# Optimization experiments

Hardware: AMD Instinct MI355X
Metric: run time of the kernel (lower is better)

The kernel has to match this reference:

```python
import jax, jax.numpy as jnp
import numpy as np

B, T, C = 2, 2048, 2048
H, D = 16, 128


def _rope(x, cos, sin):
    # x: [B,H,T,D], cos/sin: [T,D//2]
    half = x.shape[-1] // 2
    x1, x2 = x[..., :half], x[..., half:]
    c = cos[None, None, :, :]
    s = sin[None, None, :, :]
    return jnp.concatenate([x1 * c - x2 * s, x1 * s + x2 * c], axis=-1)


def setup_inputs() -> dict:
    key = jax.random.key(0)
    k1, k2, k3, k4, k5 = jax.random.split(key, 5)
    x = jax.random.normal(k1, (B, T, C), dtype=jnp.float32)
    cos = jax.random.uniform(k2, (T, D // 2), dtype=jnp.float32)
    sin = jax.random.uniform(k3, (T, D // 2), dtype=jnp.float32)
    scale = 1.0 / np.sqrt(C)
    W_qkv = jax.random.normal(k4, (C, 3 * C), dtype=jnp.float32) * scale
    W_proj = jax.random.normal(k5, (C, C), dtype=jnp.float32) * scale
    return {"x": x, "cos": cos, "sin": sin, "W_qkv": W_qkv, "W_proj": W_proj}


def reference(x, cos, sin, W_qkv, W_proj):
    Bx, Tx, Cx = x.shape
    qkv = x @ W_qkv  # [B,T,3C]
    q, k, v = jnp.split(qkv, 3, axis=-1)
    # [B,T,C] -> [B,H,T,D]
    q = q.reshape(Bx, Tx, H, D).transpose(0, 2, 1, 3)
    k = k.reshape(Bx, Tx, H, D).transpose(0, 2, 1, 3)
    v = v.reshape(Bx, Tx, H, D).transpose(0, 2, 1, 3)
    q = _rope(q, cos, sin)
    k = _rope(k, cos, sin)
    # causal SDPA
    scores = jnp.einsum("bhqd,bhkd->bhqk", q, k) / jnp.sqrt(jnp.float32(D))
    causal = jnp.tril(jnp.ones((Tx, Tx), dtype=bool))
    scores = jnp.where(causal[None, None], scores, jnp.finfo(scores.dtype).min)
    attn = jax.nn.softmax(scores, axis=-1)
    out = jnp.einsum("bhqk,bhkd->bhqd", attn, v)
    out = out.transpose(0, 2, 1, 3).reshape(Bx, Tx, Cx)
    return out @ W_proj
```

## Files before the change

### kernel.cpp

```cpp
#include <hip/hip_runtime.h>
#include <stdint.h>

#define B_  2
#define T_  2048
#define C_  2048
#define H_  16
#define D_  128
#define BH_ 32
#define M_  4096

typedef __attribute__((ext_vector_type(8))) __bf16  bf16x8;
typedef __attribute__((ext_vector_type(4))) float   floatx4;
typedef __attribute__((ext_vector_type(4))) ushort  ushortx4;

__device__ __forceinline__ ushort f2bf(float f) {
    union { float f; uint32_t u; } v; v.f = f;
    return (ushort)((v.u + 0x7fffu + ((v.u >> 16) & 1u)) >> 16);
}

__device__ __forceinline__ float bf2f(ushort u) {
    union { uint32_t u; float f; } v; v.u = ((uint32_t)u) << 16;
    return v.f;
}

__device__ __forceinline__ floatx4 mfma_bf16(bf16x8 a, bf16x8 b, floatx4 c) {
    return __builtin_amdgcn_mfma_f32_16x16x32_bf16(a, b, c, 0, 0, 0);
}

__device__ __forceinline__ void async16(const ushort* g, ushort* l) {
    __builtin_amdgcn_global_load_lds(
        (const __attribute__((address_space(1))) uint32_t*)g,
        (__attribute__((address_space(3))) uint32_t*)l, 16, 0, 0);
}

__global__ __launch_bounds__(256) void convert_bf16(
    const float* __restrict__ X, ushort* __restrict__ Xb)
{
    const int i = blockIdx.x * 256 + threadIdx.x;
    const float4 v = ((const float4*)X)[i];
    ushortx4 p = { f2bf(v.x), f2bf(v.y), f2bf(v.z), f2bf(v.w) };
    ((ushortx4*)Xb)[i] = p;
}

__global__ __launch_bounds__(256) void transpose_w(
    const float* __restrict__ W, ushort* __restrict__ Wt, int Kdim, int Ndim)
{
    __shared__ float tile[32][33];
    const int n0 = blockIdx.x * 32, k0 = blockIdx.y * 32;
    const int tx = threadIdx.x, ty = threadIdx.y;
    #pragma unroll
    for (int j = 0; j < 4; j++)
        tile[ty + j*8][tx] = W[(size_t)(k0 + ty + j*8) * Ndim + n0 + tx];
    __syncthreads();
    #pragma unroll
    for (int j = 0; j < 4; j++)
        Wt[(size_t)(n0 + ty + j*8) * Kdim + k0 + tx] = f2bf(tile[tx][ty + j*8]);
}

#define BM 128
#define BN 128
#define BK 32

__global__ __launch_bounds__(256) void gemm_bt(
    const ushort* __restrict__ A, const ushort* __restrict__ Bt,
    float* __restrict__ Co, int Ndim, int Kdim)
{
    __shared__ __align__(16) ushort As[BM * BK];
    __shared__ __align__(16) ushort Bs[BN * BK];
    const int tid  = threadIdx.x;
    const int lane = tid & 63;
    const int w    = tid >> 6;
    const int wm   = (w >> 1) * 64;
    const int wn   = (w & 1) * 64;
    const int lr   = lane & 15;
    const int quad = lane >> 4;
    const int srow = lane >> 2;
    const int soff = (lane & 3) * 8;

    const ushort* Ablk = A  + (size_t)(blockIdx.y * BM) * Kdim;
    const ushort* Bblk = Bt + (size_t)(blockIdx.x * BN) * Kdim;

    floatx4 acc[4][4];
    #pragma unroll
    for (int i = 0; i < 4; i++)
        #pragma unroll
        for (int j = 0; j < 4; j++)
            acc[i][j] = (floatx4){0.f, 0.f, 0.f, 0.f};

    for (int k0 = 0; k0 < Kdim; k0 += BK) {
        __syncthreads();
        #pragma unroll
        for (int j = 0; j < 2; j++) {
            const int row = w * 32 + j * 16 + srow;
            async16(Ablk + (size_t)row * Kdim + k0 + soff,
                    As + (w * 32 + j * 16) * BK);
            async16(Bblk + (size_t)row * Kdim + k0 + soff,
                    Bs + (w * 32 + j * 16) * BK);
        }
        __syncthreads();

        bf16x8 af[4], bfr[4];
        #pragma unroll
        for (int mi = 0; mi < 4; mi++)
            af[mi] = *(const bf16x8*)(&As[(wm + mi*16 + lr) * BK + quad * 8]);
        #pragma unroll
        for (int ni = 0; ni < 4; ni++)
            bfr[ni] = *(const bf16x8*)(&Bs[(wn + ni*16 + lr) * BK + quad * 8]);
        #pragma unroll
        for (int mi = 0; mi < 4; mi++)
            #pragma unroll
            for (int ni = 0; ni < 4; ni++)
                acc[mi][ni] = mfma_bf16(af[mi], bfr[ni], acc[mi][ni]);
    }

    const size_t row0 = (size_t)blockIdx.y * BM + wm;
    const size_t col0 = (size_t)blockIdx.x * BN + wn;
    #pragma unroll
    for (int mi = 0; mi < 4; mi++)
        #pragma unroll
        for (int ni = 0; ni < 4; ni++)
            #pragma unroll
            for (int r = 0; r < 4; r++)
                Co[(row0 + mi*16 + quad*4 + r) * (size_t)Ndim + col0 + ni*16 + lr]
                    = acc[mi][ni][r];
}

__global__ __launch_bounds__(256) void gemm_qkv(
    const ushort* __restrict__ A, const ushort* __restrict__ Bt,
    const float* __restrict__ cosb, const float* __restrict__ sinb,
    ushort* __restrict__ qb, ushort* __restrict__ kbf, ushort* __restrict__ vt)
{
    __shared__ __align__(16) ushort smem[17408];
    ushort* As = smem;
    ushort* Bs = smem + 4096;

    const int tid  = threadIdx.x;
    const int lane = tid & 63;
    const int w    = tid >> 6;
    const int wm   = (w >> 1) * 64;
    const int wn   = (w & 1) * 64;
    const int lr   = lane & 15;
    const int quad = lane >> 4;
    const int srow = lane >> 2;
    const int soff = (lane & 3) * 8;

    const int Kdim = C_;
    const ushort* Ablk = A  + (size_t)(blockIdx.y * BM) * Kdim;
    const ushort* Bblk = Bt + (size_t)(blockIdx.x * BN) * Kdim;

    floatx4 acc[4][4];
    #pragma unroll
    for (int i = 0; i < 4; i++)
        #pragma unroll
        for (int j = 0; j < 4; j++)
            acc[i][j] = (floatx4){0.f, 0.f, 0.f, 0.f};

    for (int k0 = 0; k0 < Kdim; k0 += BK) {
        __syncthreads();
        #pragma unroll
        for (int j = 0; j < 2; j++) {
            const int row = w * 32 + j * 16 + srow;
            async16(Ablk + (size_t)row * Kdim + k0 + soff,
                    As + (w * 32 + j * 16) * BK);
            async16(Bblk + (size_t)row * Kdim + k0 + soff,
                    Bs + (w * 32 + j * 16) * BK);
        }
        __syncthreads();

        bf16x8 af[4], bfr[4];
        #pragma unroll
        for (int mi = 0; mi < 4; mi++)
            af[mi] = *(const bf16x8*)(&As[(wm + mi*16 + lr) * BK + quad * 8]);
        #pragma unroll
        for (int ni = 0; ni < 4; ni++)
            bfr[ni] = *(const bf16x8*)(&Bs[(wn + ni*16 + lr) * BK + quad * 8]);
        #pragma unroll
        for (int mi = 0; mi < 4; mi++)
            #pragma unroll
            for (int ni = 0; ni < 4; ni++)
                acc[mi][ni] = mfma_bf16(af[mi], bfr[ni], acc[mi][ni]);
    }

    const int h   = blockIdx.x & 15;
    const int qt  = blockIdx.x >> 4;
    const int b   = blockIdx.y >> 4;
    const int t0g = (blockIdx.y & 15) * 128;
    const int bh  = b * 16 + h;

    __syncthreads();

    if (qt < 2) {
        #pragma unroll
        for (int mi = 0; mi < 4; mi++)
            #pragma unroll
            for (int ni = 0; ni < 4; ni++)
                #pragma unroll
                for (int r = 0; r < 4; r++) {
                    const int t = wm + mi*16 + quad*4 + r;
                    const int d = wn + ni*16 + lr;
                    smem[t * 136 + d] = f2bf(acc[mi][ni][r]);
                }
        __syncthreads();

        const int t  = tid >> 1;
        const int c0 = (tid & 1) * 32;
        bf16x8 x1v[4], x2v[4];
        #pragma unroll
        for (int u = 0; u < 4; u++) {
            x1v[u] = *(const bf16x8*)(smem + t * 136 + c0 + u * 8);
            x2v[u] = *(const bf16x8*)(smem + t * 136 + 64 + c0 + u * 8);
        }
        const float4* cp4 = (const float4*)(cosb + (size_t)(t0g + t) * 64 + c0);
        const float4* sp4 = (const float4*)(sinb + (size_t)(t0g + t) * 64 + c0);
        ushort* outp = (qt == 0 ? qb : kbf) + ((size_t)bh * T_ + t0g + t) * D_;
        #pragma unroll
        for (int u = 0; u < 4; u++) {
            float cc[8], ss[8];
            *(float4*)(cc)     = cp4[u * 2];
            *(float4*)(cc + 4) = cp4[u * 2 + 1];
            *(float4*)(ss)     = sp4[u * 2];
            *(float4*)(ss + 4) = sp4[u * 2 + 1];
            ushortx4 lo0, lo1, hi0, hi1;
            #pragma unroll
            for (int e = 0; e < 8; e++) {
                const float x1 = (float)x1v[u][e];
                const float x2 = (float)x2v[u][e];
                const ushort vlo = f2bf(x1 * cc[e] - x2 * ss[e]);
                const ushort vhi = f2bf(x1 * ss[e] + x2 * cc[e]);
                if (e < 4) { lo0[e] = vlo; hi0[e] = vhi; }
                else       { lo1[e-4] = vlo; hi1[e-4] = vhi; }
            }
            *(ushortx4*)(outp + c0 + u*8)          = lo0;
            *(ushortx4*)(outp + c0 + u*8 + 4)      = lo1;
            *(ushortx4*)(outp + 64 + c0 + u*8)     = hi0;
            *(ushortx4*)(outp + 64 + c0 + u*8 + 4) = hi1;
        }
    } else {
        #pragma unroll
        for (int mi = 0; mi < 4; mi++)
            #pragma unroll
            for (int ni = 0; ni < 4; ni++)
                #pragma unroll
                for (int r = 0; r < 4; r++) {
                    const int t = wm + mi*16 + quad*4 + r;
                    const int d = wn + ni*16 + lr;
                    smem[d * 128 + (t & 7) + 8 * ((t >> 3) ^ (d & 15))]
                        = f2bf(acc[mi][ni][r]);
                }
        __syncthreads();

        const int d    = tid >> 1;
        const int half = tid & 1;
        ushort* outp = vt + ((size_t)bh * D_ + d) * T_ + t0g + half * 64;
        #pragma unroll
        for (int u = 0; u < 8; u++) {
            const int gu = half * 8 + u;
            bf16x8 vv = *(const bf16x8*)(smem + d * 128 + 8 * (gu ^ (d & 15)));
            *(bf16x8*)(outp + u * 8) = vv;
        }
    }
}

__global__ __launch_bounds__(256, 2) void flash_attn(
    const ushort* __restrict__ qb, const ushort* __restrict__ kb,
    const ushort* __restrict__ vt, ushort* __restrict__ attnoutb)
{
    __shared__ __align__(16) ushort kt_s[2][64 * 128];
    __shared__ __align__(16) ushort vt_s[2][128 * 64];
    __shared__ __align__(16) ushort pl_s[4][16 * 40];

    const int w    = threadIdx.x >> 6;
    const int lane = threadIdx.x & 63;
    const int lr   = lane & 15;
    const int quad = lane >> 4;

    const int bh = blockIdx.x & 31;
    const int m  = 31 - (blockIdx.x >> 5);
    const int qt = 4 * m + w;
    const int qbase = qt * 16;
    const int nk = m + 1;
    const int bb = bh >> 4, hh = bh & 15;

    const ushort* kbp = kb + (size_t)bh * T_ * D_;
    const ushort* vbp = vt + (size_t)bh * D_ * T_;
    ushort* pl = pl_s[w];

    const int krow4 = lane >> 4;
    const int kunit = lane & 15;
    const int vrow8 = lane >> 3;
    const int vunit = lane & 7;

    bf16x8 qf[4];
    const ushort* qrow = qb + ((size_t)bh * T_ + qbase + lr) * D_ + quad * 8;
    #pragma unroll
    for (int kc = 0; kc < 4; kc++)
        qf[kc] = *(const bf16x8*)(qrow + kc * 32);

    floatx4 o[8];
    #pragma unroll
    for (int dc = 0; dc < 8; dc++) o[dc] = (floatx4){0.f, 0.f, 0.f, 0.f};
    floatx4 lac = (floatx4){0.f, 0.f, 0.f, 0.f};

    const __bf16 one = (__bf16)1.0f;
    const bf16x8 ones = {one, one, one, one, one, one, one, one};
    const float SCL  = 0.08838834764831845f * 1.4426950408889634f;
    const float BIAS = 23.083120654223414f;

    {
        const int kb0 = 0;
        #pragma unroll
        for (int j = 0; j < 4; j++) {
            const int row = w * 16 + j * 4 + krow4;
            const ushort* gp = kbp + (size_t)(kb0 + row) * D_
                                   + ((kunit ^ (row & 15)) << 3);
            async16(gp, kt_s[0] + (w * 16 + j * 4) * 128);
        }
        #pragma unroll
        for (int j = 0; j < 4; j++) {
            const int row = w * 32 + j * 8 + vrow8;
            const ushort* gp = vbp + (size_t)row * T_ + kb0
                                   + ((vunit ^ (row & 7)) << 3);
            async16(gp, vt_s[0] + (w * 32 + j * 8) * 64);
        }
    }
    __syncthreads();

    for (int kt = 0; kt < nk; ++kt) {
        const int bsel = kt & 1;
        const int kb0  = kt * 64;

        if (kt + 1 < nk) {
            const int kb1 = kb0 + 64;
            #pragma unroll
            for (int j = 0; j < 4; j++) {
                const int row = w * 16 + j * 4 + krow4;
                const ushort* gp = kbp + (size_t)(kb1 + row) * D_
                                       + ((kunit ^ (row & 15)) << 3);
                async16(gp, kt_s[bsel ^ 1] + (w * 16 + j * 4) * 128);
            }
            #pragma unroll
            for (int j = 0; j < 4; j++) {
                const int row = w * 32 + j * 8 + vrow8;
                const ushort* gp = vbp + (size_t)row * T_ + kb1
                                       + ((vunit ^ (row & 7)) << 3);
                async16(gp, vt_s[bsel ^ 1] + (w * 32 + j * 8) * 64);
            }
        }

        const ushort* kbuf = kt_s[bsel];
        const ushort* vbuf = vt_s[bsel];

        #pragma unroll
        for (int half = 0; half < 2; ++half) {
            floatx4 st[2];
            #pragma unroll
            for (int jj = 0; jj < 2; ++jj) {
                const int j = half * 2 + jj;
                floatx4 s = (floatx4){0.f, 0.f, 0.f, 0.f};
                const int kl = j * 16 + lr;
                #pragma unroll
                for (int kc = 0; kc < 4; kc++) {
                    bf16x8 af = *(const bf16x8*)(
                        kbuf + kl * 128 + ((((kc << 2) | quad) ^ lr) << 3));
                    s = mfma_bf16(af, qf[kc], s);
                }
                st[jj] = s;
            }
            #pragma unroll
            for (int jj = 0; jj < 2; ++jj) {
                const int j = half * 2 + jj;
                const int kg0 = kb0 + j * 16 + quad * 4;
                float p[4];
                #pragma unroll
                for (int r = 0; r < 4; r++) {
                    float e = __builtin_amdgcn_exp2f(fmaf(st[jj][r], SCL, -BIAS));
                    p[r] = (kg0 + r > qbase + lr) ? 0.f : e;
                }
                uint2 pk;
                pk.x = (uint32_t)f2bf(p[0]) | ((uint32_t)f2bf(p[1]) << 16);
                pk.y = (uint32_t)f2bf(p[2]) | ((uint32_t)f2bf(p[3]) << 16);
                *(uint2*)(pl + lr * 40 + jj * 16 + quad * 4) = pk;
            }
            bf16x8 pf = *(const bf16x8*)(pl + lr * 40 + quad * 8);
            lac = mfma_bf16(pf, ones, lac);
            #pragma unroll
            for (int dc = 0; dc < 8; dc++) {
                const int d = dc * 16 + lr;
                bf16x8 vf = *(const bf16x8*)(
                    vbuf + d * 64 + ((((half << 2) | quad) ^ (lr & 7)) << 3));
                o[dc] = mfma_bf16(pf, vf, o[dc]);
            }
        }

        __syncthreads();
    }

    #pragma unroll
    for (int dc = 0; dc < 8; dc++)
        #pragma unroll
        for (int r = 0; r < 4; r++) {
            const int trow = qbase + quad * 4 + r;
            attnoutb[((size_t)(bb * T_ + trow)) * C_ + hh * D_ + dc * 16 + lr]
                = f2bf(o[dc][r] / lac[r]);
        }
}

extern "C" void kernel_launch(void* const* d_in, const int* in_sizes, int n_in,
                              void* d_out, int out_size, void* d_ws, size_t ws_size,
                              hipStream_t stream)
{
    (void)in_sizes; (void)n_in; (void)out_size; (void)ws_size;
    const float* x     = (const float*)d_in[0];
    const float* cosb  = (const float*)d_in[1];
    const float* sinb  = (const float*)d_in[2];
    const float* Wqkv  = (const float*)d_in[3];
    const float* Wproj = (const float*)d_in[4];
    float* out = (float*)d_out;

    char* ws = (char*)d_ws;
    ushort* xb       = (ushort*)(ws);
    ushort* Wtq      = (ushort*)(ws + 16777216);
    ushort* Wtp      = (ushort*)(ws + 41943040);
    ushort* qb       = (ushort*)(ws + 50331648);
    ushort* kbf      = (ushort*)(ws + 67108864);
    ushort* vt       = (ushort*)(ws + 83886080);
    ushort* attnoutb = (ushort*)(ws + 100663296);

    dim3 tb32(32, 8);
    transpose_w<<<dim3(3 * C_ / 32, C_ / 32), tb32, 0, stream>>>(Wqkv, Wtq, C_, 3 * C_);
    transpose_w<<<dim3(C_ / 32, C_ / 32),     tb32, 0, stream>>>(Wproj, Wtp, C_, C_);
    convert_bf16<<<(M_ * C_ / 4) / 256, 256, 0, stream>>>(x, xb);

    gemm_qkv<<<dim3(3 * C_ / BN, M_ / BM), 256, 0, stream>>>(
        xb, Wtq, cosb, sinb, qb, kbf, vt);

    flash_attn<<<BH_ * 32, 256, 0, stream>>>(qb, kbf, vt, attnoutb);

    gemm_bt<<<dim3(C_ / BN, M_ / BM), 256, 0, stream>>>(attnoutb, Wtp, out, C_, C_);
}
```

Baseline: 406.4 us.

## Process two query sub-tiles per warp in flash attention, halving grid size

Each warp now handles two 16-row query tiles (32 rows per warp, 128 per block), so every K/V fragment read from shared memory feeds two MFMAs and each block loads K/V tiles for twice as many queries. The grid shrinks from 1024 to 512 blocks, and a per-warp guard skips key tiles that lie entirely above the causal diagonal for that warp. Block ordering is changed to interleave large and small causal workloads. Register pressure roughly doubles for accumulators, which may hurt occupancy under the 2-blocks-per-CU launch bound, and fewer blocks reduce parallelism.

```diff
diff --git a/kernel.cpp b/kernel.cpp
--- a/kernel.cpp
+++ b/kernel.cpp
@@ -267,7 +267,7 @@
 {
     __shared__ __align__(16) ushort kt_s[2][64 * 128];
     __shared__ __align__(16) ushort vt_s[2][128 * 64];
-    __shared__ __align__(16) ushort pl_s[4][16 * 40];
+    __shared__ __align__(16) ushort pl_s[4][2][16 * 40];
 
     const int w    = threadIdx.x >> 6;
     const int lane = threadIdx.x & 63;
@@ -275,31 +275,42 @@
     const int quad = lane >> 4;
 
     const int bh = blockIdx.x & 31;
-    const int m  = 31 - (blockIdx.x >> 5);
-    const int qt = 4 * m + w;
-    const int qbase = qt * 16;
-    const int nk = m + 1;
+    const int zz = blockIdx.x >> 5;
+    const int mm = (zz < 8) ? (15 - zz) : (zz - 8);
+    const int qbase0 = mm * 128 + w * 32;
+    const int qbase1 = qbase0 + 16;
+    const int nk = 2 * mm + 2;
     const int bb = bh >> 4, hh = bh & 15;
 
     const ushort* kbp = kb + (size_t)bh * T_ * D_;
     const ushort* vbp = vt + (size_t)bh * D_ * T_;
-    ushort* pl = pl_s[w];
+    ushort* pl0 = pl_s[w][0];
+    ushort* pl1 = pl_s[w][1];
 
     const int krow4 = lane >> 4;
     const int kunit = lane & 15;
     const int vrow8 = lane >> 3;
     const int vunit = lane & 7;
 
-    bf16x8 qf[4];
-    const ushort* qrow = qb + ((size_t)bh * T_ + qbase + lr) * D_ + quad * 8;
-    #pragma unroll
-    for (int kc = 0; kc < 4; kc++)
-        qf[kc] = *(const bf16x8*)(qrow + kc * 32);
-
-    floatx4 o[8];
-    #pragma unroll
-    for (int dc = 0; dc < 8; dc++) o[dc] = (floatx4){0.f, 0.f, 0.f, 0.f};
-    floatx4 lac = (floatx4){0.f, 0.f, 0.f, 0.f};
+    bf16x8 qf0[4], qf1[4];
+    {
+        const ushort* qrow0 = qb + ((size_t)bh * T_ + qbase0 + lr) * D_ + quad * 8;
+        const ushort* qrow1 = qb + ((size_t)bh * T_ + qbase1 + lr) * D_ + quad * 8;
+        #pragma unroll
+        for (int kc = 0; kc < 4; kc++) {
+            qf0[kc] = *(const bf16x8*)(qrow0 + kc * 32);
+            qf1[kc] = *(const bf16x8*)(qrow1 + kc * 32);
+        }
+    }
+
+    floatx4 o0[8], o1[8];
+    #pragma unroll
+    for (int dc = 0; dc < 8; dc++) {
+        o0[dc] = (floatx4){0.f, 0.f, 0.f, 0.f};
+        o1[dc] = (floatx4){0.f, 0.f, 0.f, 0.f};
+    }
+    floatx4 lac0 = (floatx4){0.f, 0.f, 0.f, 0.f};
+    floatx4 lac1 = (floatx4){0.f, 0.f, 0.f, 0.f};
 
     const __bf16 one = (__bf16)1.0f;
     const bf16x8 ones = {one, one, one, one, one, one, one, one};
@@ -307,18 +318,17 @@
     const float BIAS = 23.083120654223414f;
 
     {
-        const int kb0 = 0;
         #pragma unroll
         for (int j = 0; j < 4; j++) {
             const int row = w * 16 + j * 4 + krow4;
-            const ushort* gp = kbp + (size_t)(kb0 + row) * D_
+            const ushort* gp = kbp + (size_t)row * D_
                                    + ((kunit ^ (row & 15)) << 3);
             async16(gp, kt_s[0] + (w * 16 + j * 4) * 128);
         }
         #pragma unroll
         for (int j = 0; j < 4; j++) {
             const int row = w * 32 + j * 8 + vrow8;
-            const ushort* gp = vbp + (size_t)row * T_ + kb0
+            const ushort* gp = vbp + (size_t)row * T_
                                    + ((vunit ^ (row & 7)) << 3);
             async16(gp, vt_s[0] + (w * 32 + j * 8) * 64);
         }
@@ -347,49 +357,61 @@
             }
         }
 
-        const ushort* kbuf = kt_s[bsel];
-        const ushort* vbuf = vt_s[bsel];
-
-        #pragma unroll
-        for (int half = 0; half < 2; ++half) {
-            floatx4 st[2];
-            #pragma unroll
-            for (int jj = 0; jj < 2; ++jj) {
-                const int j = half * 2 + jj;
-                floatx4 s = (floatx4){0.f, 0.f, 0.f, 0.f};
-                const int kl = j * 16 + lr;
+        if (kb0 <= qbase0 + 31) {
+            const ushort* kbuf = kt_s[bsel];
+            const ushort* vbuf = vt_s[bsel];
+
+            #pragma unroll
+            for (int half = 0; half < 2; ++half) {
+                floatx4 st0[2], st1[2];
                 #pragma unroll
-                for (int kc = 0; kc < 4; kc++) {
-                    bf16x8 af = *(const bf16x8*)(
-                        kbuf + kl * 128 + ((((kc << 2) | quad) ^ lr) << 3));
-                    s = mfma_bf16(af, qf[kc], s);
+                for (int jj = 0; jj < 2; ++jj) {
+                    const int j = half * 2 + jj;
+                    floatx4 s0 = (floatx4){0.f, 0.f, 0.f, 0.f};
+                    floatx4 s1 = (floatx4){0.f, 0.f, 0.f, 0.f};
+                    const int kl = j * 16 + lr;
+                    #pragma unroll
+                    for (int kc = 0; kc < 4; kc++) {
+                        bf16x8 af = *(const bf16x8*)(
+                            kbuf + kl * 128 + ((((kc << 2) | quad) ^ lr) << 3));
+                        s0 = mfma_bf16(af, qf0[kc], s0);
+                        s1 = mfma_bf16(af, qf1[kc], s1);
+                    }
+                    st0[jj] = s0;
+                    st1[jj] = s1;
                 }
-                st[jj] = s;
+                #pragma unroll
+                for (int jj = 0; jj < 2; ++jj) {
+                    const int kg0 = kb0 + (half * 2 + jj) * 16 + quad * 4;
+                    float p0[4], p1[4];
+                    #pragma unroll
+                    for (int r = 0; r < 4; r++) {
+                        float e0 = __builtin_amdgcn_exp2f(fmaf(st0[jj][r], SCL, -BIAS));
+                        float e1 = __builtin_amdgcn_exp2f(fmaf(st1[jj][r], SCL, -BIAS));
+                        p0[r] = (kg0 + r > qbase0 + lr) ? 0.f : e0;
+                        p1[r] = (kg0 + r > qbase1 + lr) ? 0.f : e1;
+                    }
+                    uint2 pk0, pk1;
+                    pk0.x = (uint32_t)f2bf(p0[0]) | ((uint32_t)f2bf(p0[1]) << 16);
+                    pk0.y = (uint32_t)f2bf(p0[2]) | ((uint32_t)f2bf(p0[3]) << 16);
+                    pk1.x = (uint32_t)f2bf(p1[0]) | ((uint32_t)f2bf(p1[1]) << 16);
+                    pk1.y = (uint32_t)f2bf(p1[2]) | ((uint32_t)f2bf(p1[3]) << 16);
+                    *(uint2*)(pl0 + lr * 40 + jj * 16 + quad * 4) = pk0;
+                    *(uint2*)(pl1 + lr * 40 + jj * 16 + quad * 4) = pk1;
+                }
+                bf16x8 pf0 = *(const bf16x8*)(pl0 + lr * 40 + quad * 8);
+                bf16x8 pf1 = *(const bf16x8*)(pl1 + lr * 40 + quad * 8);
+                lac0 = mfma_bf16(pf0, ones, lac0);
+                lac1 = mfma_bf16(pf1, ones, lac1);
+                #pragma unroll
+                for (int dc = 0; dc < 8; dc++) {
+                    const int d = dc * 16 + lr;
+                    bf16x8 vf = *(const bf16x8*)(
+                        vbuf + d * 64 + ((((half << 2) | quad) ^ (lr & 7)) << 3));
+                    o0[dc] = mfma_bf16(pf0, vf, o0[dc]);
+                    o1[dc] = mfma_bf16(pf1, vf, o1[dc]);
+                }
             }
-            #pragma unroll
-            for (int jj = 0; jj < 2; ++jj) {
-                const int j = half * 2 + jj;
-                const int kg0 = kb0 + j * 16 + quad * 4;
-                float p[4];
-                #pragma unroll
-                for (int r = 0; r < 4; r++) {
-                    float e = __builtin_amdgcn_exp2f(fmaf(st[jj][r], SCL, -BIAS));
-                    p[r] = (kg0 + r > qbase + lr) ? 0.f : e;
-                }
-                uint2 pk;
-                pk.x = (uint32_t)f2bf(p[0]) | ((uint32_t)f2bf(p[1]) << 16);
-                pk.y = (uint32_t)f2bf(p[2]) | ((uint32_t)f2bf(p[3]) << 16);
-                *(uint2*)(pl + lr * 40 + jj * 16 + quad * 4) = pk;
-            }
-            bf16x8 pf = *(const bf16x8*)(pl + lr * 40 + quad * 8);
-            lac = mfma_bf16(pf, ones, lac);
-            #pragma unroll
-            for (int dc = 0; dc < 8; dc++) {
-                const int d = dc * 16 + lr;
-                bf16x8 vf = *(const bf16x8*)(
-                    vbuf + d * 64 + ((((half << 2) | quad) ^ (lr & 7)) << 3));
-                o[dc] = mfma_bf16(pf, vf, o[dc]);
-            }
         }
 
         __syncthreads();
@@ -399,9 +421,12 @@
     for (int dc = 0; dc < 8; dc++)
         #pragma unroll
         for (int r = 0; r < 4; r++) {
-            const int trow = qbase + quad * 4 + r;
-            attnoutb[((size_t)(bb * T_ + trow)) * C_ + hh * D_ + dc * 16 + lr]
-                = f2bf(o[dc][r] / lac[r]);
+            const int trow0 = qbase0 + quad * 4 + r;
+            const int trow1 = qbase1 + quad * 4 + r;
+            attnoutb[((size_t)(bb * T_ + trow0)) * C_ + hh * D_ + dc * 16 + lr]
+                = f2bf(o0[dc][r] / lac0[r]);
+            attnoutb[((size_t)(bb * T_ + trow1)) * C_ + hh * D_ + dc * 16 + lr]
+                = f2bf(o1[dc][r] / lac1[r]);
         }
 }
 
@@ -434,7 +459,7 @@
     gemm_qkv<<<dim3(3 * C_ / BN, M_ / BM), 256, 0, stream>>>(
         xb, Wtq, cosb, sinb, qb, kbf, vt);
 
-    flash_attn<<<BH_ * 32, 256, 0, stream>>>(qb, kbf, vt, attnoutb);
+    flash_attn<<<BH_ * 16, 256, 0, stream>>>(qb, kbf, vt, attnoutb);
 
     gemm_bt<<<dim3(C_ / BN, M_ / BM), 256, 0, stream>>>(attnoutb, Wtp, out, C_, C_);
 }
```

Result: slower. 426.4 us (+4.9%).

## Double-buffer GEMM K-loop with async prefetch two tiles ahead

Applied to the files above, without the earlier changes.

Factors the shared GEMM main loop of gemm_bt and gemm_qkv into a helper that uses two LDS buffers, issuing the async global-to-LDS loads for tile t+2 while MFMAs run on tile t. Explicit vmcnt waits, sched barriers and raised wave priority around the MFMA block replace the two __syncthreads per iteration. The goal is to hide global-load latency in the projection GEMMs, at the cost of doubled LDS for gemm_bt and hand-tuned waitcnt logic that must stay correct.

```diff
diff --git a/kernel.cpp b/kernel.cpp
--- a/kernel.cpp
+++ b/kernel.cpp
@@ -61,13 +61,24 @@
 #define BN 128
 #define BK 32
 
-__global__ __launch_bounds__(256) void gemm_bt(
-    const ushort* __restrict__ A, const ushort* __restrict__ Bt,
-    float* __restrict__ Co, int Ndim, int Kdim)
-{
-    __shared__ __align__(16) ushort As[BM * BK];
-    __shared__ __align__(16) ushort Bs[BN * BK];
-    const int tid  = threadIdx.x;
+__device__ __forceinline__ void stage_tile(
+    const ushort* __restrict__ Ablk, const ushort* __restrict__ Bblk,
+    ushort* smem, int off, int k0, int w, int srow, int soff, int Kdim)
+{
+    #pragma unroll
+    for (int j = 0; j < 2; j++) {
+        const int row = w * 32 + j * 16 + srow;
+        async16(Ablk + (size_t)row * Kdim + k0 + soff,
+                smem + off + (w * 32 + j * 16) * BK);
+        async16(Bblk + (size_t)row * Kdim + k0 + soff,
+                smem + off + 4096 + (w * 32 + j * 16) * BK);
+    }
+}
+
+__device__ __forceinline__ void kloop128(
+    const ushort* __restrict__ Ablk, const ushort* __restrict__ Bblk,
+    ushort* smem, floatx4 (&acc)[4][4], int tid, int Kdim)
+{
     const int lane = tid & 63;
     const int w    = tid >> 6;
     const int wm   = (w >> 1) * 64;
@@ -77,27 +88,18 @@
     const int srow = lane >> 2;
     const int soff = (lane & 3) * 8;
 
-    const ushort* Ablk = A  + (size_t)(blockIdx.y * BM) * Kdim;
-    const ushort* Bblk = Bt + (size_t)(blockIdx.x * BN) * Kdim;
-
-    floatx4 acc[4][4];
-    #pragma unroll
-    for (int i = 0; i < 4; i++)
-        #pragma unroll
-        for (int j = 0; j < 4; j++)
-            acc[i][j] = (floatx4){0.f, 0.f, 0.f, 0.f};
-
-    for (int k0 = 0; k0 < Kdim; k0 += BK) {
-        __syncthreads();
-        #pragma unroll
-        for (int j = 0; j < 2; j++) {
-            const int row = w * 32 + j * 16 + srow;
-            async16(Ablk + (size_t)row * Kdim + k0 + soff,
-                    As + (w * 32 + j * 16) * BK);
-            async16(Bblk + (size_t)row * Kdim + k0 + soff,
-                    Bs + (w * 32 + j * 16) * BK);
-        }
-        __syncthreads();
+    stage_tile(Ablk, Bblk, smem, 0,    0,  w, srow, soff, Kdim);
+    stage_tile(Ablk, Bblk, smem, 8192, BK, w, srow, soff, Kdim);
+    asm volatile("s_waitcnt vmcnt(4)" ::: "memory");
+    __builtin_amdgcn_sched_barrier(0);
+    __builtin_amdgcn_s_barrier();
+
+    const int niter = Kdim / BK;
+    #pragma unroll 2
+    for (int t = 0; t < niter; ++t) {
+        const int off = (t & 1) << 13;
+        const ushort* As = smem + off;
+        const ushort* Bs = smem + off + 4096;
 
         bf16x8 af[4], bfr[4];
         #pragma unroll
@@ -106,34 +108,35 @@
         #pragma unroll
         for (int ni = 0; ni < 4; ni++)
             bfr[ni] = *(const bf16x8*)(&Bs[(wn + ni*16 + lr) * BK + quad * 8]);
+        asm volatile("s_waitcnt lgkmcnt(0)" ::: "memory");
+        __builtin_amdgcn_sched_barrier(0);
+        __builtin_amdgcn_s_setprio(1);
         #pragma unroll
         for (int mi = 0; mi < 4; mi++)
             #pragma unroll
             for (int ni = 0; ni < 4; ni++)
                 acc[mi][ni] = mfma_bf16(af[mi], bfr[ni], acc[mi][ni]);
+        __builtin_amdgcn_s_setprio(0);
+
+        __builtin_amdgcn_s_barrier();
+
+        const int k2 = (t + 2) * BK;
+        if (k2 < Kdim) {
+            stage_tile(Ablk, Bblk, smem, off, k2, w, srow, soff, Kdim);
+            asm volatile("s_waitcnt vmcnt(4)" ::: "memory");
+        } else {
+            asm volatile("s_waitcnt vmcnt(0)" ::: "memory");
+        }
+        __builtin_amdgcn_sched_barrier(0);
+        __builtin_amdgcn_s_barrier();
     }
-
-    const size_t row0 = (size_t)blockIdx.y * BM + wm;
-    const size_t col0 = (size_t)blockIdx.x * BN + wn;
-    #pragma unroll
-    for (int mi = 0; mi < 4; mi++)
-        #pragma unroll
-        for (int ni = 0; ni < 4; ni++)
-            #pragma unroll
-            for (int r = 0; r < 4; r++)
-                Co[(row0 + mi*16 + quad*4 + r) * (size_t)Ndim + col0 + ni*16 + lr]
-                    = acc[mi][ni][r];
-}
-
-__global__ __launch_bounds__(256) void gemm_qkv(
+}
+
+__global__ __launch_bounds__(256) void gemm_bt(
     const ushort* __restrict__ A, const ushort* __restrict__ Bt,
-    const float* __restrict__ cosb, const float* __restrict__ sinb,
-    ushort* __restrict__ qb, ushort* __restrict__ kbf, ushort* __restrict__ vt)
-{
-    __shared__ __align__(16) ushort smem[17408];
-    ushort* As = smem;
-    ushort* Bs = smem + 4096;
-
+    float* __restrict__ Co, int Ndim, int Kdim)
+{
+    __shared__ __align__(16) ushort smem[16384];
     const int tid  = threadIdx.x;
     const int lane = tid & 63;
     const int w    = tid >> 6;
@@ -141,8 +144,45 @@
     const int wn   = (w & 1) * 64;
     const int lr   = lane & 15;
     const int quad = lane >> 4;
-    const int srow = lane >> 2;
-    const int soff = (lane & 3) * 8;
+
+    const ushort* Ablk = A  + (size_t)(blockIdx.y * BM) * Kdim;
+    const ushort* Bblk = Bt + (size_t)(blockIdx.x * BN) * Kdim;
+
+    floatx4 acc[4][4];
+    #pragma unroll
+    for (int i = 0; i < 4; i++)
+        #pragma unroll
+        for (int j = 0; j < 4; j++)
+            acc[i][j] = (floatx4){0.f, 0.f, 0.f, 0.f};
+
+    kloop128(Ablk, Bblk, smem, acc, tid, Kdim);
+
+    const size_t row0 = (size_t)blockIdx.y * BM + wm;
+    const size_t col0 = (size_t)blockIdx.x * BN + wn;
+    #pragma unroll
+    for (int mi = 0; mi < 4; mi++)
+        #pragma unroll
+        for (int ni = 0; ni < 4; ni++)
+            #pragma unroll
+            for (int r = 0; r < 4; r++)
+                Co[(row0 + mi*16 + quad*4 + r) * (size_t)Ndim + col0 + ni*16 + lr]
+                    = acc[mi][ni][r];
+}
+
+__global__ __launch_bounds__(256) void gemm_qkv(
+    const ushort* __restrict__ A, const ushort* __restrict__ Bt,
+    const float* __restrict__ cosb, const float* __restrict__ sinb,
+    ushort* __restrict__ qb, ushort* __restrict__ kbf, ushort* __restrict__ vt)
+{
+    __shared__ __align__(16) ushort smem[17408];
+
+    const int tid  = threadIdx.x;
+    const int lane = tid & 63;
+    const int w    = tid >> 6;
+    const int wm   = (w >> 1) * 64;
+    const int wn   = (w & 1) * 64;
+    const int lr   = lane & 15;
+    const int quad = lane >> 4;
 
     const int Kdim = C_;
     const ushort* Ablk = A  + (size_t)(blockIdx.y * BM) * Kdim;
@@ -155,31 +195,7 @@
         for (int j = 0; j < 4; j++)
             acc[i][j] = (floatx4){0.f, 0.f, 0.f, 0.f};
 
-    for (int k0 = 0; k0 < Kdim; k0 += BK) {
-        __syncthreads();
-        #pragma unroll
-        for (int j = 0; j < 2; j++) {
-            const int row = w * 32 + j * 16 + srow;
-            async16(Ablk + (size_t)row * Kdim + k0 + soff,
-                    As + (w * 32 + j * 16) * BK);
-            async16(Bblk + (size_t)row * Kdim + k0 + soff,
-                    Bs + (w * 32 + j * 16) * BK);
-        }
-        __syncthreads();
-
-        bf16x8 af[4], bfr[4];
-        #pragma unroll
-        for (int mi = 0; mi < 4; mi++)
-            af[mi] = *(const bf16x8*)(&As[(wm + mi*16 + lr) * BK + quad * 8]);
-        #pragma unroll
-        for (int ni = 0; ni < 4; ni++)
-            bfr[ni] = *(const bf16x8*)(&Bs[(wn + ni*16 + lr) * BK + quad * 8]);
-        #pragma unroll
-        for (int mi = 0; mi < 4; mi++)
-            #pragma unroll
-            for (int ni = 0; ni < 4; ni++)
-                acc[mi][ni] = mfma_bf16(af[mi], bfr[ni], acc[mi][ni]);
-    }
+    kloop128(Ablk, Bblk, smem, acc, tid, Kdim);
 
     const int h   = blockIdx.x & 15;
     const int qt  = blockIdx.x >> 4;
@@ -355,9 +371,9 @@
             floatx4 st[2];
             #pragma unroll
             for (int jj = 0; jj < 2; ++jj) {
-                const int j = half * 2 + jj;
+                const int jx = half * 2 + jj;
                 floatx4 s = (floatx4){0.f, 0.f, 0.f, 0.f};
-                const int kl = j * 16 + lr;
+                const int kl = jx * 16 + lr;
                 #pragma unroll
                 for (int kc = 0; kc < 4; kc++) {
                     bf16x8 af = *(const bf16x8*)(
@@ -368,8 +384,7 @@
             }
             #pragma unroll
             for (int jj = 0; jj < 2; ++jj) {
-                const int j = half * 2 + jj;
-                const int kg0 = kb0 + j * 16 + quad * 4;
+                const int kg0 = kb0 + (half * 2 + jj) * 16 + quad * 4;
                 float p[4];
                 #pragma unroll
                 for (int r = 0; r < 4; r++) {
```

Measured after the change: 383.1 us. 5.7% less time.
